# Kernel optimization log

Hardware: AMD Instinct MI355X
Metric: run time of the kernel (lower is better)

Reference implementation:

```python
import jax, jax.numpy as jnp
import numpy as np

RESOLUTION = 128


def _bin_mask():
    # [4, 2] bool: corner i, dim d -> True if corner uses floor coord in dim d
    neigs = jnp.arange(4, dtype=jnp.int32)[:, None]
    dims = jnp.arange(2, dtype=jnp.int32)[None, :]
    return (neigs & (1 << dims)) == 0


def setup_inputs() -> dict:
    key = jax.random.key(0)
    k1, k2 = jax.random.split(key)
    batch = 65536
    res, map_num, feat_dim = RESOLUTION, 128, 8
    inputs = jax.random.uniform(k1, (batch, 2), dtype=jnp.float32)
    # xavier_uniform over [res^2, map_num*feat_dim]
    fan_in, fan_out = res * res, map_num * feat_dim
    bound = float(np.sqrt(6.0 / (fan_in + fan_out)))
    embeddings = jax.random.uniform(k2, (res * res, map_num * feat_dim),
                                    dtype=jnp.float32, minval=-bound, maxval=bound)
    return {"inputs": inputs, "embeddings": embeddings}


def reference(inputs, embeddings):
    res = RESOLUTION
    bin_mask = _bin_mask()                      # [4, 2]
    x = inputs * (res - 1)                      # [B, 2]
    xi = jnp.floor(x).astype(jnp.int32)         # [B, 2]
    xf = x - jax.lax.stop_gradient(jnp.floor(x))  # fractional part, grads flow via x
    xi = xi[:, None, :]                         # [B, 1, 2]
    xf = xf[:, None, :]                         # [B, 1, 2]
    neigs = jnp.where(bin_mask, xi, xi + 1)     # [B, 4, 2]
    ids = neigs[..., 0] * res + neigs[..., 1]   # [B, 4]
    neigs_features = embeddings[ids]            # [B, 4, D] irregular gather
    weights = jnp.where(bin_mask, 1.0 - xf, xf) # [B, 4, 2]
    w = jnp.prod(weights, axis=-1, keepdims=True)  # [B, 4, 1]
    return jnp.sum(neigs_features * w, axis=-2)    # [B, D]
```

## Files before the change

kernel.cpp:

```cpp
#include <hip/hip_runtime.h>

#define RES  128
#define FEAT 1024

__global__ __launch_bounds__(256)
void DenseMap_kernel(const float* __restrict__ inputs,
                     const float* __restrict__ emb,
                     float* __restrict__ out)
{
    const int p = blockIdx.x;
    const int c = threadIdx.x;

    const float x0 = inputs[2 * p + 0] * (float)(RES - 1);
    const float x1 = inputs[2 * p + 1] * (float)(RES - 1);
    const float f0 = floorf(x0);
    const float f1 = floorf(x1);
    const int   i0 = (int)f0;
    const int   i1 = (int)f1;
    const float xf0 = x0 - f0;
    const float xf1 = x1 - f1;

    const float w00 = (1.0f - xf0) * (1.0f - xf1);
    const float w01 = (1.0f - xf0) * xf1;
    const float w10 = xf0 * (1.0f - xf1);
    const float w11 = xf0 * xf1;

    const long base = (long)(i0 * RES + i1) * FEAT;
    const float4* e00 = (const float4*)(emb + base) + c;
    const float4* e01 = (const float4*)(emb + base + FEAT) + c;
    const float4* e10 = (const float4*)(emb + base + (long)RES * FEAT) + c;
    const float4* e11 = (const float4*)(emb + base + (long)RES * FEAT + FEAT) + c;

    const float4 a = *e00;
    const float4 b = *e01;
    const float4 g = *e10;
    const float4 h = *e11;

    float4 r;
    r.x = a.x * w00 + b.x * w01 + g.x * w10 + h.x * w11;
    r.y = a.y * w00 + b.y * w01 + g.y * w10 + h.y * w11;
    r.z = a.z * w00 + b.z * w01 + g.z * w10 + h.z * w11;
    r.w = a.w * w00 + b.w * w01 + g.w * w10 + h.w * w11;

    ((float4*)(out + (long)p * FEAT))[c] = r;
}

extern "C" void kernel_launch(void* const* d_in, const int* in_sizes, int n_in,
                              void* d_out, int out_size, void* d_ws, size_t ws_size,
                              hipStream_t stream)
{
    const float* inputs = (const float*)d_in[0];
    const float* emb    = (const float*)d_in[1];
    float*       out    = (float*)d_out;

    const int batch = in_sizes[0] / 2;
    DenseMap_kernel<<<batch, 256, 0, stream>>>(inputs, emb, out);
}
```

Baseline: 428.5 us.

## Sort points by grid cell and swizzle blocks across XCDs for cache reuse

Adds a counting sort (histogram, scan, scatter) that orders batch points by their floor cell, then processes them in sorted order with four points per block. A block index swizzle groups contiguous sorted chunks onto the same XCD so that neighbouring cells share embedding rows in L2. This is meant to cut repeated gather traffic for the 4 KB embedding rows. It adds several small kernel launches, atomics and a single-block scan, and leaves a fallback for when the workspace is too small.

```diff
diff --git a/kernel.cpp b/kernel.cpp
--- a/kernel.cpp
+++ b/kernel.cpp
@@ -1,12 +1,101 @@
 #include <hip/hip_runtime.h>
 
-#define RES  128
-#define FEAT 1024
+#define RES   128
+#define FEAT  1024
+#define NBINS (RES * RES)
 
 __global__ __launch_bounds__(256)
-void DenseMap_kernel(const float* __restrict__ inputs,
-                     const float* __restrict__ emb,
-                     float* __restrict__ out)
+void hist_kernel(const float* __restrict__ inputs, unsigned* __restrict__ hist, int N)
+{
+    int p = blockIdx.x * 256 + threadIdx.x;
+    if (p >= N) return;
+    int i0 = (int)floorf(inputs[2 * p + 0] * (float)(RES - 1));
+    int i1 = (int)floorf(inputs[2 * p + 1] * (float)(RES - 1));
+    atomicAdd(&hist[i0 * RES + i1], 1u);
+}
+
+__global__ __launch_bounds__(256)
+void scan_kernel(unsigned* __restrict__ hist)
+{
+    __shared__ unsigned part[256];
+    int t = threadIdx.x;
+    int base = t * 64;
+    unsigned s = 0;
+    for (int k = 0; k < 64; ++k) s += hist[base + k];
+    part[t] = s;
+    __syncthreads();
+    if (t == 0) {
+        unsigned run = 0;
+        for (int i = 0; i < 256; ++i) { unsigned v = part[i]; part[i] = run; run += v; }
+    }
+    __syncthreads();
+    unsigned run = part[t];
+    for (int k = 0; k < 64; ++k) { unsigned v = hist[base + k]; hist[base + k] = run; run += v; }
+}
+
+__global__ __launch_bounds__(256)
+void scatter_kernel(const float* __restrict__ inputs, unsigned* __restrict__ hist,
+                    unsigned* __restrict__ order, int N)
+{
+    int p = blockIdx.x * 256 + threadIdx.x;
+    if (p >= N) return;
+    int i0 = (int)floorf(inputs[2 * p + 0] * (float)(RES - 1));
+    int i1 = (int)floorf(inputs[2 * p + 1] * (float)(RES - 1));
+    unsigned pos = atomicAdd(&hist[i0 * RES + i1], 1u);
+    order[pos] = (unsigned)p;
+}
+
+__global__ __launch_bounds__(256)
+void DenseMap_sorted_kernel(const float* __restrict__ inputs,
+                            const float* __restrict__ emb,
+                            const unsigned* __restrict__ order,
+                            float* __restrict__ out,
+                            int N, int chunk)
+{
+    const int b = blockIdx.x;
+    const int c = threadIdx.x;
+    const int g = (chunk > 0) ? ((b & 7) * chunk + (b >> 3)) : b;
+
+#pragma unroll
+    for (int j = 0; j < 4; ++j) {
+        const int s = g * 4 + j;
+        if (s >= N) break;
+        const int p = (int)order[s];
+
+        const float x0 = inputs[2 * p + 0] * (float)(RES - 1);
+        const float x1 = inputs[2 * p + 1] * (float)(RES - 1);
+        const float f0 = floorf(x0);
+        const float f1 = floorf(x1);
+        const int   i0 = (int)f0;
+        const int   i1 = (int)f1;
+        const float xf0 = x0 - f0;
+        const float xf1 = x1 - f1;
+
+        const float w00 = (1.0f - xf0) * (1.0f - xf1);
+        const float w01 = (1.0f - xf0) * xf1;
+        const float w10 = xf0 * (1.0f - xf1);
+        const float w11 = xf0 * xf1;
+
+        const long base = (long)(i0 * RES + i1) * FEAT;
+        const float4 a = ((const float4*)(emb + base))[c];
+        const float4 bb = ((const float4*)(emb + base + FEAT))[c];
+        const float4 gg = ((const float4*)(emb + base + (long)RES * FEAT))[c];
+        const float4 h = ((const float4*)(emb + base + (long)RES * FEAT + FEAT))[c];
+
+        float4 r;
+        r.x = a.x * w00 + bb.x * w01 + gg.x * w10 + h.x * w11;
+        r.y = a.y * w00 + bb.y * w01 + gg.y * w10 + h.y * w11;
+        r.z = a.z * w00 + bb.z * w01 + gg.z * w10 + h.z * w11;
+        r.w = a.w * w00 + bb.w * w01 + gg.w * w10 + h.w * w11;
+
+        ((float4*)(out + (long)p * FEAT))[c] = r;
+    }
+}
+
+__global__ __launch_bounds__(256)
+void DenseMap_fallback_kernel(const float* __restrict__ inputs,
+                              const float* __restrict__ emb,
+                              float* __restrict__ out)
 {
     const int p = blockIdx.x;
     const int c = threadIdx.x;
@@ -26,15 +115,10 @@
     const float w11 = xf0 * xf1;
 
     const long base = (long)(i0 * RES + i1) * FEAT;
-    const float4* e00 = (const float4*)(emb + base) + c;
-    const float4* e01 = (const float4*)(emb + base + FEAT) + c;
-    const float4* e10 = (const float4*)(emb + base + (long)RES * FEAT) + c;
-    const float4* e11 = (const float4*)(emb + base + (long)RES * FEAT + FEAT) + c;
-
-    const float4 a = *e00;
-    const float4 b = *e01;
-    const float4 g = *e10;
-    const float4 h = *e11;
+    const float4 a = ((const float4*)(emb + base))[c];
+    const float4 b = ((const float4*)(emb + base + FEAT))[c];
+    const float4 g = ((const float4*)(emb + base + (long)RES * FEAT))[c];
+    const float4 h = ((const float4*)(emb + base + (long)RES * FEAT + FEAT))[c];
 
     float4 r;
     r.x = a.x * w00 + b.x * w01 + g.x * w10 + h.x * w11;
@@ -53,6 +137,22 @@
     const float* emb    = (const float*)d_in[1];
     float*       out    = (float*)d_out;
 
-    const int batch = in_sizes[0] / 2;
-    DenseMap_kernel<<<batch, 256, 0, stream>>>(inputs, emb, out);
+    const int N = in_sizes[0] / 2;
+    const size_t need = (size_t)(NBINS + N) * sizeof(unsigned);
+
+    if (ws_size >= need) {
+        unsigned* hist  = (unsigned*)d_ws;
+        unsigned* order = hist + NBINS;
+
+        hipMemsetAsync(hist, 0, NBINS * sizeof(unsigned), stream);
+        hist_kernel<<<(N + 255) / 256, 256, 0, stream>>>(inputs, hist, N);
+        scan_kernel<<<1, 256, 0, stream>>>(hist);
+        scatter_kernel<<<(N + 255) / 256, 256, 0, stream>>>(inputs, hist, order, N);
+
+        const int G = (N + 3) / 4;
+        const int chunk = (G % 8 == 0) ? (G / 8) : 0;
+        DenseMap_sorted_kernel<<<G, 256, 0, stream>>>(inputs, emb, order, out, N, chunk);
+    } else {
+        DenseMap_fallback_kernel<<<N, 256, 0, stream>>>(inputs, emb, out);
+    }
 }
```

New measurement: 388.6 us. 9.3% less time.
